# Kernel tuning notes

Hardware: AMD Instinct MI355X
Metric: run time of the kernel (lower is better)

Reference implementation:

```python
import jax, jax.numpy as jnp
import numpy as np

D_MODEL = 1024
D_STATE = 16
D_CONV = 4
EXPAND = 2
D_INNER = EXPAND * D_MODEL          # 2048
DT_RANK = D_INNER // 16             # 128
BATCH = 2
SEQLEN = 1024


def _silu(x):
    return x * jax.nn.sigmoid(x)


def setup_inputs() -> dict:
    key = jax.random.key(0)
    ks = jax.random.split(key, 8)
    s = 0.02
    A_init = jnp.tile(jnp.arange(1, D_STATE + 1, dtype=jnp.float32)[None, :], (D_INNER, 1))
    return {
        "x": jax.random.normal(ks[0], (BATCH, SEQLEN, D_MODEL), jnp.float32),
        "W_in": jax.random.normal(ks[1], (D_MODEL, 2 * D_INNER), jnp.float32) * s,
        "conv_k": jax.random.normal(ks[2], (D_CONV, 1, D_INNER), jnp.float32) * s,  # (kw, in/groups, out)
        "conv_b": jnp.zeros((D_INNER,), jnp.float32),
        "W_xproj": jax.random.normal(ks[3], (D_INNER, DT_RANK + 2 * D_STATE), jnp.float32) * s,
        "W_dt": jax.random.normal(ks[4], (DT_RANK, D_INNER), jnp.float32) * s,
        "b_dt": jnp.zeros((D_INNER,), jnp.float32),
        "A_log": jnp.log(A_init),
        "D": jnp.ones((D_INNER,), jnp.float32),
        "W_out": jax.random.normal(ks[5], (D_INNER, D_MODEL), jnp.float32) * s,
    }


def reference(x, W_in, conv_k, conv_b, W_xproj, W_dt, b_dt, A_log, D, W_out):
    # in_proj and gate split
    xz = x @ W_in                                   # (B, L, 2*Di)
    x_in, z = jnp.split(xz, 2, axis=-1)             # each (B, L, Di)

    # depthwise causal conv1d: left-pad by d_conv-1 (keras padding='causal')
    xp = jnp.pad(x_in, ((0, 0), (D_CONV - 1, 0), (0, 0)))
    x_in = jax.lax.conv_general_dilated(
        xp, conv_k, window_strides=(1,), padding='VALID',
        dimension_numbers=('NWC', 'WIO', 'NWC'),
        feature_group_count=D_INNER) + conv_b
    u = _silu(x_in)                                 # (B, L, Di)

    # input-dependent SSM params
    x_dbl = u @ W_xproj                             # (B, L, dt_rank + 2*N)
    dt_low, Bm, Cm = jnp.split(x_dbl, [DT_RANK, DT_RANK + D_STATE], axis=-1)
    dt = jax.nn.softplus(dt_low @ W_dt + b_dt)      # (B, L, Di)
    A = -jnp.exp(A_log)                             # (Di, N)
    dA = jnp.exp(jnp.einsum('bld,dn->bldn', dt, A)) # (B, L, Di, N)
    dB = jnp.einsum('bld,bln->bldn', dt, Bm)        # (B, L, Di, N)

    # selective scan over sequence length
    def step(h, e):
        a_t, b_t, u_t, c_t = e                      # (B,Di,N), (B,Di,N), (B,Di), (B,N)
        h = a_t * h + b_t * u_t[..., None]
        y_t = jnp.einsum('bdn,bn->bd', h, c_t)
        return h, y_t

    h0 = jnp.zeros((x.shape[0], D_INNER, D_STATE), dtype=x.dtype)
    xs = (jnp.swapaxes(dA, 0, 1), jnp.swapaxes(dB, 0, 1),
          jnp.swapaxes(u, 0, 1), jnp.swapaxes(Cm, 0, 1))
    _, yT = jax.lax.scan(step, h0, xs)              # (L, B, Di)
    y = jnp.swapaxes(yT, 0, 1) + u * D              # skip connection

    return (y * _silu(z)) @ W_out                   # (B, L, d_model)
```

## Files before the change

### kernel.cpp

```cpp
#include <hip/hip_runtime.h>
#include <hip/hip_bf16.h>

#define D_MODEL 1024
#define D_STATE 16
#define D_CONV 4
#define D_INNER 2048
#define DT_RANK 128
#define BATCH 2
#define SEQLEN 1024
#define XCOLS 160
#define NCHUNK 64
#define LCHUNK 16

typedef __hip_bfloat16 bf16;
typedef __attribute__((ext_vector_type(8))) short short8;
typedef __attribute__((ext_vector_type(4))) float f32x4;

__device__ __forceinline__ unsigned short f2bf_bits(float f) {
    bf16 h = __float2bfloat16(f);
    return *(unsigned short*)&h;
}


__global__ __launch_bounds__(256)
void convert_f32_bf16(const float* __restrict__ src, bf16* __restrict__ dst, int n)
{
    int i = blockIdx.x * 256 + threadIdx.x;
    if (i < n) dst[i] = __float2bfloat16(src[i]);
}

__global__ __launch_bounds__(256)
void transpose_f32_bf16(const float* __restrict__ B, bf16* __restrict__ Bt,
                        int K, int N)
{
    __shared__ float t[32][33];
    const int tx = threadIdx.x & 31, ty = threadIdx.x >> 5;
    const int n0 = blockIdx.x * 32, k0 = blockIdx.y * 32;
    #pragma unroll
    for (int r = 0; r < 4; ++r) {
        int k = k0 + ty + r * 8;
        int n = n0 + tx;
        t[ty + r * 8][tx] = (n < N) ? B[(size_t)k * N + n] : 0.f;
    }
    __syncthreads();
    #pragma unroll
    for (int r = 0; r < 4; ++r) {
        int n = n0 + ty + r * 8;
        int k = k0 + tx;
        Bt[(size_t)n * K + k] = __float2bfloat16(t[tx][ty + r * 8]);
    }
}

__global__ __launch_bounds__(256)
void gemm_mfma_bt(const bf16* __restrict__ A, const bf16* __restrict__ Bt,
                  float* __restrict__ C, int M, int N, int K, int ldc, int kchunk)
{
    __shared__ short As[128 * 32];
    __shared__ short Bs[128 * 32];
    const int tid = threadIdx.x;
    const int lane = tid & 63, wave = tid >> 6;
    const int wm = (wave >> 1) * 64, wn = (wave & 1) * 64;
    const int row0 = blockIdx.y * 128, col0 = blockIdx.x * 128;
    const int r_m = lane & 15, r_q = lane >> 4;
    const int kstart = blockIdx.z * kchunk;
    float* Cz = C + (size_t)blockIdx.z * M * ldc;

    const int srow = tid >> 2, schk = (tid & 3) * 8;
    const uint4* Ag0 = (const uint4*)(A  + (size_t)(row0 + srow)      * K + kstart + schk);
    const uint4* Ag1 = (const uint4*)(A  + (size_t)(row0 + srow + 64) * K + kstart + schk);
    const uint4* Bg0 = (const uint4*)(Bt + (size_t)(col0 + srow)      * K + kstart + schk);
    const uint4* Bg1 = (const uint4*)(Bt + (size_t)(col0 + srow + 64) * K + kstart + schk);
    uint4* AsW0 = (uint4*)&As[srow * 32 + schk];
    uint4* AsW1 = (uint4*)&As[(srow + 64) * 32 + schk];
    uint4* BsW0 = (uint4*)&Bs[srow * 32 + schk];
    uint4* BsW1 = (uint4*)&Bs[(srow + 64) * 32 + schk];

    f32x4 acc[4][4];
    #pragma unroll
    for (int i = 0; i < 4; ++i)
        #pragma unroll
        for (int j = 0; j < 4; ++j)
            #pragma unroll
            for (int r = 0; r < 4; ++r) acc[i][j][r] = 0.f;

    for (int k0 = 0; k0 < kchunk; k0 += 32) {
        const int kq = k0 >> 3;
        uint4 a0 = Ag0[kq], a1 = Ag1[kq], b0 = Bg0[kq], b1 = Bg1[kq];
        __syncthreads();
        *AsW0 = a0; *AsW1 = a1; *BsW0 = b0; *BsW1 = b1;
        __syncthreads();
        short8 af[4], bfr[4];
        #pragma unroll
        for (int i = 0; i < 4; ++i)
            af[i] = *(const short8*)&As[(wm + i * 16 + r_m) * 32 + r_q * 8];
        #pragma unroll
        for (int j = 0; j < 4; ++j)
            bfr[j] = *(const short8*)&Bs[(wn + j * 16 + r_m) * 32 + r_q * 8];
        #pragma unroll
        for (int i = 0; i < 4; ++i)
            #pragma unroll
            for (int j = 0; j < 4; ++j)
                acc[i][j] = __builtin_amdgcn_mfma_f32_16x16x32_bf16(
                    af[i], bfr[j], acc[i][j], 0, 0, 0);
    }

    #pragma unroll
    for (int i = 0; i < 4; ++i) {
        #pragma unroll
        for (int j = 0; j < 4; ++j) {
            int row = row0 + wm + i * 16 + r_q * 4;
            int col = col0 + wn + j * 16 + r_m;
            if (col < N) {
                #pragma unroll
                for (int r = 0; r < 4; ++r)
                    Cz[(size_t)(row + r) * ldc + col] = acc[i][j][r];
            }
        }
    }
}

__global__ __launch_bounds__(256)
void reduce_xdbl(const float* __restrict__ Cpart, float* __restrict__ x_dbl,
                 bf16* __restrict__ dtA_bf)
{
    int i = blockIdx.x * 256 + threadIdx.x;
    if (i >= 2048 * XCOLS) return;
    int r = i / XCOLS, c = i - r * XCOLS;
    float s = 0.f;
    #pragma unroll
    for (int z = 0; z < 8; ++z)
        s += Cpart[(size_t)z * 2048 * 256 + (size_t)r * 256 + c];
    x_dbl[i] = s;
    if (c < DT_RANK) dtA_bf[(size_t)r * DT_RANK + c] = __float2bfloat16(s);
}

__global__ __launch_bounds__(256)
void reduce_out(const float* __restrict__ Cpart, float* __restrict__ out)
{
    int i = blockIdx.x * 256 + threadIdx.x;
    const float4* p0 = (const float4*)Cpart;
    const float4* p1 = p0 + (size_t)2048 * 1024 / 4;
    float4 a = p0[i], b = p1[i];
    float4 r; r.x = a.x + b.x; r.y = a.y + b.y; r.z = a.z + b.z; r.w = a.w + b.w;
    ((float4*)out)[i] = r;
}

__global__ __launch_bounds__(256)
void conv_silu_kernel(const float* __restrict__ xz,
                      const float* __restrict__ conv_k,
                      const float* __restrict__ conv_b,
                      float* __restrict__ u, bf16* __restrict__ u_bf)
{
    int idx4 = blockIdx.x * 256 + threadIdx.x;
    int d4 = idx4 & (D_INNER / 4 - 1);
    int t = (idx4 >> 9) & (SEQLEN - 1);
    int b = idx4 >> 19;
    float4 acc = ((const float4*)conv_b)[d4];
    #pragma unroll
    for (int k = 0; k < D_CONV; ++k) {
        int tt = t + k - (D_CONV - 1);
        if (tt >= 0) {
            float4 xv = ((const float4*)xz)[(size_t)(b * SEQLEN + tt) * (2 * D_INNER / 4) + d4];
            float4 kv = ((const float4*)conv_k)[k * (D_INNER / 4) + d4];
            acc.x = fmaf(xv.x, kv.x, acc.x);
            acc.y = fmaf(xv.y, kv.y, acc.y);
            acc.z = fmaf(xv.z, kv.z, acc.z);
            acc.w = fmaf(xv.w, kv.w, acc.w);
        }
    }
    float4 uv;
    uv.x = acc.x / (1.f + __expf(-acc.x));
    uv.y = acc.y / (1.f + __expf(-acc.y));
    uv.z = acc.z / (1.f + __expf(-acc.z));
    uv.w = acc.w / (1.f + __expf(-acc.w));
    ((float4*)u)[idx4] = uv;
    ushort4 pk;
    pk.x = f2bf_bits(uv.x); pk.y = f2bf_bits(uv.y);
    pk.z = f2bf_bits(uv.z); pk.w = f2bf_bits(uv.w);
    ((ushort4*)u_bf)[idx4] = pk;
}

__device__ __forceinline__ float softplus_f(float x) {
    return fmaxf(x, 0.f) + __logf(1.f + __expf(-fabsf(x)));
}

__global__ __launch_bounds__(256)
void scan_phase1(const float* __restrict__ dt_pre,
                 const float* __restrict__ b_dt,
                 const float* __restrict__ A_log,
                 const float* __restrict__ u,
                 const float* __restrict__ x_dbl,
                 float* __restrict__ Pst, float* __restrict__ Sst)
{
    __shared__ float Bsm[LCHUNK][16];
    const int d = blockIdx.x * 256 + threadIdx.x;
    const int c = blockIdx.y, b = blockIdx.z;
    const int t0 = c * LCHUNK;
    {
        int tt = threadIdx.x >> 4, n = threadIdx.x & 15;
        Bsm[tt][n] = x_dbl[(size_t)(b * SEQLEN + t0 + tt) * XCOLS + DT_RANK + n];
    }
    float A_row[D_STATE];
    #pragma unroll
    for (int n = 0; n < D_STATE; ++n)
        A_row[n] = -__expf(A_log[d * D_STATE + n]);
    const float bdt = b_dt[d];
    __syncthreads();
    float P[D_STATE], S[D_STATE];
    #pragma unroll
    for (int n = 0; n < D_STATE; ++n) { P[n] = 1.f; S[n] = 0.f; }
    const float* dpp = dt_pre + (size_t)(b * SEQLEN + t0) * D_INNER + d;
    const float* upp = u + (size_t)(b * SEQLEN + t0) * D_INNER + d;
    #pragma unroll
    for (int t = 0; t < LCHUNK; ++t) {
        float xv = dpp[(size_t)t * D_INNER] + bdt;
        float dtv = softplus_f(xv);
        float du = dtv * upp[(size_t)t * D_INNER];
        const float4* b4 = (const float4*)&Bsm[t][0];
        #pragma unroll
        for (int q = 0; q < 4; ++q) {
            float4 v = b4[q];
            float Bn[4] = {v.x, v.y, v.z, v.w};
            #pragma unroll
            for (int e = 0; e < 4; ++e) {
                int n = q * 4 + e;
                float a = __expf(dtv * A_row[n]);
                P[n] *= a;
                S[n] = fmaf(a, S[n], du * Bn[e]);
            }
        }
    }
    const size_t base = ((size_t)(b * NCHUNK + c) * D_STATE) * D_INNER + d;
    #pragma unroll
    for (int n = 0; n < D_STATE; ++n) {
        Pst[base + (size_t)n * D_INNER] = P[n];
        Sst[base + (size_t)n * D_INNER] = S[n];
    }
}

__global__ __launch_bounds__(256)
void scan_phase2(const float* __restrict__ Pst, float* __restrict__ Sst)
{
    const int d = blockIdx.x * 256 + threadIdx.x;
    const int n = blockIdx.y;
    const int b = blockIdx.z;
    float h = 0.f;
    for (int c = 0; c < NCHUNK; ++c) {
        const size_t idx = ((size_t)(b * NCHUNK + c) * D_STATE + n) * D_INNER + d;
        float Pv = Pst[idx], Sv = Sst[idx];
        Sst[idx] = h;
        h = fmaf(Pv, h, Sv);
    }
}

__global__ __launch_bounds__(256)
void scan_phase3(const float* __restrict__ dt_pre,
                 const float* __restrict__ b_dt,
                 const float* __restrict__ A_log,
                 const float* __restrict__ u,
                 const float* __restrict__ x_dbl,
                 const float* __restrict__ Dvec,
                 const float* __restrict__ xz,
                 const float* __restrict__ hin,
                 bf16* __restrict__ g_bf)
{
    __shared__ float BCs[LCHUNK][32];
    const int d = blockIdx.x * 256 + threadIdx.x;
    const int c = blockIdx.y, b = blockIdx.z;
    const int t0 = c * LCHUNK;
    {
        int i0 = threadIdx.x;
        int tt = i0 >> 5, col = i0 & 31;
        BCs[tt][col] = x_dbl[(size_t)(b * SEQLEN + t0 + tt) * XCOLS + DT_RANK + col];
        int i1 = i0 + 256;
        tt = i1 >> 5; col = i1 & 31;
        BCs[tt][col] = x_dbl[(size_t)(b * SEQLEN + t0 + tt) * XCOLS + DT_RANK + col];
    }
    float A_row[D_STATE];
    #pragma unroll
    for (int n = 0; n < D_STATE; ++n)
        A_row[n] = -__expf(A_log[d * D_STATE + n]);
    const float bdt = b_dt[d];
    const float Dd = Dvec[d];
    __syncthreads();
    float h[D_STATE];
    const size_t base = ((size_t)(b * NCHUNK + c) * D_STATE) * D_INNER + d;
    #pragma unroll
    for (int n = 0; n < D_STATE; ++n) h[n] = hin[base + (size_t)n * D_INNER];
    const float* dpp = dt_pre + (size_t)(b * SEQLEN + t0) * D_INNER + d;
    const float* upp = u + (size_t)(b * SEQLEN + t0) * D_INNER + d;
    const float* zpp = xz + (size_t)(b * SEQLEN + t0) * (2 * D_INNER) + D_INNER + d;
    bf16* gpp = g_bf + (size_t)(b * SEQLEN + t0) * D_INNER + d;
    #pragma unroll
    for (int t = 0; t < LCHUNK; ++t) {
        float xv = dpp[(size_t)t * D_INNER] + bdt;
        float dtv = softplus_f(xv);
        float uv = upp[(size_t)t * D_INNER];
        float zv = zpp[(size_t)t * 2 * D_INNER];
        float du = dtv * uv;
        float y = 0.f;
        const float4* bc4 = (const float4*)&BCs[t][0];
        #pragma unroll
        for (int q = 0; q < 4; ++q) {
            float4 v = bc4[q];
            float4 w = bc4[q + 4];
            float Bn[4] = {v.x, v.y, v.z, v.w};
            float Cn[4] = {w.x, w.y, w.z, w.w};
            #pragma unroll
            for (int e = 0; e < 4; ++e) {
                int n = q * 4 + e;
                float a = __expf(dtv * A_row[n]);
                h[n] = fmaf(a, h[n], du * Bn[e]);
                y = fmaf(h[n], Cn[e], y);
            }
        }
        float gy = y + uv * Dd;
        float sz = zv / (1.f + __expf(-zv));
        gpp[(size_t)t * D_INNER] = __float2bfloat16(gy * sz);
    }
}

extern "C" void kernel_launch(void* const* d_in, const int* in_sizes, int n_in,
                              void* d_out, int out_size, void* d_ws, size_t ws_size,
                              hipStream_t stream)
{
    const float* x      = (const float*)d_in[0];
    const float* W_in   = (const float*)d_in[1];
    const float* conv_k = (const float*)d_in[2];
    const float* conv_b = (const float*)d_in[3];
    const float* W_xproj= (const float*)d_in[4];
    const float* W_dt   = (const float*)d_in[5];
    const float* b_dt   = (const float*)d_in[6];
    const float* A_log  = (const float*)d_in[7];
    const float* Dvec   = (const float*)d_in[8];
    const float* W_out  = (const float*)d_in[9];
    float* out = (float*)d_out;

    const int BL = BATCH * SEQLEN;

    float* ws     = (float*)d_ws;
    float* xz     = ws;
    float* u      = xz     + (size_t)BL * 2 * D_INNER;
    float* x_dbl  = u      + (size_t)BL * D_INNER;
    float* dt_pre = x_dbl  + (size_t)BL * XCOLS;
    float* Pst    = dt_pre + (size_t)BL * D_INNER;
    float* Sst    = Pst    + (size_t)BATCH * NCHUNK * D_STATE * D_INNER;
    float* Cpart3 = Pst;
    float* Cpart6 = Pst;
    bf16*  x_bf   = (bf16*)Sst;
    bf16* Win_t  = (bf16*)(Sst + (size_t)BATCH * NCHUNK * D_STATE * D_INNER);
    bf16* u_bf   = Win_t + (size_t)4096 * 1024;
    bf16* Wxp_t  = u_bf  + (size_t)BL * D_INNER;
    bf16* dtA_bf = Wxp_t + (size_t)256 * 2048;
    bf16* Wdt_t  = dtA_bf+ (size_t)BL * DT_RANK;
    bf16* g_bf   = Wdt_t + (size_t)2048 * 128;
    bf16* Wout_t = g_bf  + (size_t)BL * D_INNER;

    convert_f32_bf16<<<(BL * D_MODEL) / 256, 256, 0, stream>>>(x, x_bf, BL * D_MODEL);
    transpose_f32_bf16<<<dim3(4096 / 32, 1024 / 32), 256, 0, stream>>>(W_in, Win_t, D_MODEL, 2 * D_INNER);
    transpose_f32_bf16<<<dim3(256 / 32, 2048 / 32), 256, 0, stream>>>(W_xproj, Wxp_t, D_INNER, XCOLS);
    transpose_f32_bf16<<<dim3(2048 / 32, 128 / 32), 256, 0, stream>>>(W_dt, Wdt_t, DT_RANK, D_INNER);
    transpose_f32_bf16<<<dim3(1024 / 32, 2048 / 32), 256, 0, stream>>>(W_out, Wout_t, D_INNER, D_MODEL);

    gemm_mfma_bt<<<dim3(32, 16, 1), 256, 0, stream>>>(
        x_bf, Win_t, xz, BL, 2 * D_INNER, D_MODEL, 2 * D_INNER, D_MODEL);

    conv_silu_kernel<<<(BL * D_INNER / 4) / 256, 256, 0, stream>>>(xz, conv_k, conv_b, u, u_bf);

    gemm_mfma_bt<<<dim3(2, 16, 8), 256, 0, stream>>>(
        u_bf, Wxp_t, Cpart3, BL, 256, D_INNER, 256, 256);
    reduce_xdbl<<<(BL * XCOLS + 255) / 256, 256, 0, stream>>>(Cpart3, x_dbl, dtA_bf);

    gemm_mfma_bt<<<dim3(16, 16, 1), 256, 0, stream>>>(
        dtA_bf, Wdt_t, dt_pre, BL, D_INNER, DT_RANK, D_INNER, DT_RANK);

    scan_phase1<<<dim3(D_INNER / 256, NCHUNK, BATCH), 256, 0, stream>>>(
        dt_pre, b_dt, A_log, u, x_dbl, Pst, Sst);
    scan_phase2<<<dim3(D_INNER / 256, D_STATE, BATCH), 256, 0, stream>>>(Pst, Sst);
    scan_phase3<<<dim3(D_INNER / 256, NCHUNK, BATCH), 256, 0, stream>>>(
        dt_pre, b_dt, A_log, u, x_dbl, Dvec, xz, Sst, g_bf);

    gemm_mfma_bt<<<dim3(8, 16, 2), 256, 0, stream>>>(
        g_bf, Wout_t, Cpart6, BL, D_MODEL, D_INNER, D_MODEL, D_MODEL);
    reduce_out<<<(BL * D_MODEL / 4) / 256, 256, 0, stream>>>(Cpart6, out);
}
```

Before: 259.9 us.

## Fuse prep kernels, add softplus GEMM epilogue, direct-to-LDS loads, bf16 u

Merges the input conversion and four weight transposes into one prep kernel that also precomputes -exp(A_log). The dt GEMM now applies the bias and softplus in its epilogue, so the two scan phases no longer recompute them. The GEMMs stage tiles through global_load_lds straight into LDS instead of going through registers. The fp32 copy of u is dropped and the scans read the bf16 u, cutting memory traffic at some precision cost. The new LDS layout writes 8*tid contiguously while the fragment reads assume a row-by-chunk layout; these match because each row takes four 8-element chunks.

```diff
diff --git a/kernel.cpp b/kernel.cpp
--- a/kernel.cpp
+++ b/kernel.cpp
@@ -21,39 +21,86 @@
     return *(unsigned short*)&h;
 }
 
-
-__global__ __launch_bounds__(256)
-void convert_f32_bf16(const float* __restrict__ src, bf16* __restrict__ dst, int n)
-{
-    int i = blockIdx.x * 256 + threadIdx.x;
-    if (i < n) dst[i] = __float2bfloat16(src[i]);
-}
-
-__global__ __launch_bounds__(256)
-void transpose_f32_bf16(const float* __restrict__ B, bf16* __restrict__ Bt,
-                        int K, int N)
+__device__ __forceinline__ float softplus_f(float x) {
+    return fmaxf(x, 0.f) + __logf(1.f + __expf(-fabsf(x)));
+}
+
+__device__ __forceinline__ void load16_lds(void* lds, const void* g) {
+    __builtin_amdgcn_global_load_lds(
+        (const __attribute__((address_space(1))) unsigned int*)g,
+        (__attribute__((address_space(3))) unsigned int*)lds, 16, 0, 0);
+}
+
+__device__ __forceinline__ void transpose_tile(const float* __restrict__ B,
+                                               bf16* __restrict__ Bt,
+                                               int K, int N, int nt, int kt,
+                                               float (*t)[33], int tid)
+{
+    const int tx = tid & 31, ty = tid >> 5;
+    const int n0 = nt * 32, k0 = kt * 32;
+    #pragma unroll
+    for (int r = 0; r < 4; ++r) {
+        int n = n0 + tx;
+        t[ty + r * 8][tx] = (n < N) ? B[(size_t)(k0 + ty + r * 8) * N + n] : 0.f;
+    }
+    __syncthreads();
+    #pragma unroll
+    for (int r = 0; r < 4; ++r)
+        Bt[(size_t)(n0 + ty + r * 8) * K + k0 + tx] = __float2bfloat16(t[tx][ty + r * 8]);
+}
+
+__global__ __launch_bounds__(256)
+void prep_kernel(const float* __restrict__ x, bf16* __restrict__ x_bf,
+                 const float* __restrict__ W_in, bf16* __restrict__ Win_t,
+                 const float* __restrict__ W_xproj, bf16* __restrict__ Wxp_t,
+                 const float* __restrict__ W_dt, bf16* __restrict__ Wdt_t,
+                 const float* __restrict__ W_out, bf16* __restrict__ Wout_t,
+                 const float* __restrict__ A_log, float* __restrict__ Aneg)
 {
     __shared__ float t[32][33];
-    const int tx = threadIdx.x & 31, ty = threadIdx.x >> 5;
-    const int n0 = blockIdx.x * 32, k0 = blockIdx.y * 32;
-    #pragma unroll
-    for (int r = 0; r < 4; ++r) {
-        int k = k0 + ty + r * 8;
-        int n = n0 + tx;
-        t[ty + r * 8][tx] = (n < N) ? B[(size_t)k * N + n] : 0.f;
-    }
-    __syncthreads();
-    #pragma unroll
-    for (int r = 0; r < 4; ++r) {
-        int n = n0 + ty + r * 8;
-        int k = k0 + tx;
-        Bt[(size_t)n * K + k] = __float2bfloat16(t[tx][ty + r * 8]);
-    }
-}
-
+    const int tid = threadIdx.x;
+    int blk = blockIdx.x;
+    if (blk < 4096) {
+        transpose_tile(W_in, Win_t, D_MODEL, 2 * D_INNER, blk & 127, blk >> 7, t, tid);
+        return;
+    }
+    blk -= 4096;
+    if (blk < 512) {
+        transpose_tile(W_xproj, Wxp_t, D_INNER, XCOLS, blk & 7, blk >> 3, t, tid);
+        return;
+    }
+    blk -= 512;
+    if (blk < 256) {
+        transpose_tile(W_dt, Wdt_t, DT_RANK, D_INNER, blk & 63, blk >> 6, t, tid);
+        return;
+    }
+    blk -= 256;
+    if (blk < 2048) {
+        transpose_tile(W_out, Wout_t, D_INNER, D_MODEL, blk & 31, blk >> 5, t, tid);
+        return;
+    }
+    blk -= 2048;
+    if (blk < 2048) {
+        int i = blk * 256 + tid;
+        float4 v = ((const float4*)x)[i];
+        ushort4 p;
+        p.x = f2bf_bits(v.x); p.y = f2bf_bits(v.y);
+        p.z = f2bf_bits(v.z); p.w = f2bf_bits(v.w);
+        ((ushort4*)x_bf)[i] = p;
+        return;
+    }
+    blk -= 2048;
+    {
+        int i = blk * 256 + tid;
+        Aneg[i] = -__expf(A_log[i]);
+    }
+}
+
+template<int EPI>
 __global__ __launch_bounds__(256)
 void gemm_mfma_bt(const bf16* __restrict__ A, const bf16* __restrict__ Bt,
-                  float* __restrict__ C, int M, int N, int K, int ldc, int kchunk)
+                  float* __restrict__ C, const float* __restrict__ bias,
+                  int M, int N, int K, int ldc, int kchunk)
 {
     __shared__ short As[128 * 32];
     __shared__ short Bs[128 * 32];
@@ -66,14 +113,14 @@
     float* Cz = C + (size_t)blockIdx.z * M * ldc;
 
     const int srow = tid >> 2, schk = (tid & 3) * 8;
-    const uint4* Ag0 = (const uint4*)(A  + (size_t)(row0 + srow)      * K + kstart + schk);
-    const uint4* Ag1 = (const uint4*)(A  + (size_t)(row0 + srow + 64) * K + kstart + schk);
-    const uint4* Bg0 = (const uint4*)(Bt + (size_t)(col0 + srow)      * K + kstart + schk);
-    const uint4* Bg1 = (const uint4*)(Bt + (size_t)(col0 + srow + 64) * K + kstart + schk);
-    uint4* AsW0 = (uint4*)&As[srow * 32 + schk];
-    uint4* AsW1 = (uint4*)&As[(srow + 64) * 32 + schk];
-    uint4* BsW0 = (uint4*)&Bs[srow * 32 + schk];
-    uint4* BsW1 = (uint4*)&Bs[(srow + 64) * 32 + schk];
+    const bf16* Ag0 = A  + (size_t)(row0 + srow)      * K + kstart + schk;
+    const bf16* Ag1 = A  + (size_t)(row0 + srow + 64) * K + kstart + schk;
+    const bf16* Bg0 = Bt + (size_t)(col0 + srow)      * K + kstart + schk;
+    const bf16* Bg1 = Bt + (size_t)(col0 + srow + 64) * K + kstart + schk;
+    short* AsW0 = &As[8 * tid];
+    short* AsW1 = &As[8 * tid + 2048];
+    short* BsW0 = &Bs[8 * tid];
+    short* BsW1 = &Bs[8 * tid + 2048];
 
     f32x4 acc[4][4];
     #pragma unroll
@@ -84,10 +131,11 @@
             for (int r = 0; r < 4; ++r) acc[i][j][r] = 0.f;
 
     for (int k0 = 0; k0 < kchunk; k0 += 32) {
-        const int kq = k0 >> 3;
-        uint4 a0 = Ag0[kq], a1 = Ag1[kq], b0 = Bg0[kq], b1 = Bg1[kq];
         __syncthreads();
-        *AsW0 = a0; *AsW1 = a1; *BsW0 = b0; *BsW1 = b1;
+        load16_lds(AsW0, Ag0 + k0);
+        load16_lds(AsW1, Ag1 + k0);
+        load16_lds(BsW0, Bg0 + k0);
+        load16_lds(BsW1, Bg1 + k0);
         __syncthreads();
         short8 af[4], bfr[4];
         #pragma unroll
@@ -111,9 +159,17 @@
             int row = row0 + wm + i * 16 + r_q * 4;
             int col = col0 + wn + j * 16 + r_m;
             if (col < N) {
-                #pragma unroll
-                for (int r = 0; r < 4; ++r)
-                    Cz[(size_t)(row + r) * ldc + col] = acc[i][j][r];
+                if (EPI == 1) {
+                    float bv = bias[col];
+                    #pragma unroll
+                    for (int r = 0; r < 4; ++r)
+                        Cz[(size_t)(row + r) * ldc + col] =
+                            softplus_f(acc[i][j][r] + bv);
+                } else {
+                    #pragma unroll
+                    for (int r = 0; r < 4; ++r)
+                        Cz[(size_t)(row + r) * ldc + col] = acc[i][j][r];
+                }
             }
         }
     }
@@ -149,7 +205,7 @@
 void conv_silu_kernel(const float* __restrict__ xz,
                       const float* __restrict__ conv_k,
                       const float* __restrict__ conv_b,
-                      float* __restrict__ u, bf16* __restrict__ u_bf)
+                      bf16* __restrict__ u_bf)
 {
     int idx4 = blockIdx.x * 256 + threadIdx.x;
     int d4 = idx4 & (D_INNER / 4 - 1);
@@ -168,27 +224,18 @@
             acc.w = fmaf(xv.w, kv.w, acc.w);
         }
     }
-    float4 uv;
-    uv.x = acc.x / (1.f + __expf(-acc.x));
-    uv.y = acc.y / (1.f + __expf(-acc.y));
-    uv.z = acc.z / (1.f + __expf(-acc.z));
-    uv.w = acc.w / (1.f + __expf(-acc.w));
-    ((float4*)u)[idx4] = uv;
     ushort4 pk;
-    pk.x = f2bf_bits(uv.x); pk.y = f2bf_bits(uv.y);
-    pk.z = f2bf_bits(uv.z); pk.w = f2bf_bits(uv.w);
+    pk.x = f2bf_bits(acc.x / (1.f + __expf(-acc.x)));
+    pk.y = f2bf_bits(acc.y / (1.f + __expf(-acc.y)));
+    pk.z = f2bf_bits(acc.z / (1.f + __expf(-acc.z)));
+    pk.w = f2bf_bits(acc.w / (1.f + __expf(-acc.w)));
     ((ushort4*)u_bf)[idx4] = pk;
 }
 
-__device__ __forceinline__ float softplus_f(float x) {
-    return fmaxf(x, 0.f) + __logf(1.f + __expf(-fabsf(x)));
-}
-
-__global__ __launch_bounds__(256)
-void scan_phase1(const float* __restrict__ dt_pre,
-                 const float* __restrict__ b_dt,
-                 const float* __restrict__ A_log,
-                 const float* __restrict__ u,
+__global__ __launch_bounds__(256)
+void scan_phase1(const float* __restrict__ dt_s,
+                 const float* __restrict__ Aneg,
+                 const bf16* __restrict__ u_bf,
                  const float* __restrict__ x_dbl,
                  float* __restrict__ Pst, float* __restrict__ Sst)
 {
@@ -201,21 +248,22 @@
         Bsm[tt][n] = x_dbl[(size_t)(b * SEQLEN + t0 + tt) * XCOLS + DT_RANK + n];
     }
     float A_row[D_STATE];
-    #pragma unroll
-    for (int n = 0; n < D_STATE; ++n)
-        A_row[n] = -__expf(A_log[d * D_STATE + n]);
-    const float bdt = b_dt[d];
+    const float4* a4 = (const float4*)(Aneg + d * D_STATE);
+    #pragma unroll
+    for (int q = 0; q < 4; ++q) {
+        float4 v = a4[q];
+        A_row[q*4+0] = v.x; A_row[q*4+1] = v.y; A_row[q*4+2] = v.z; A_row[q*4+3] = v.w;
+    }
     __syncthreads();
     float P[D_STATE], S[D_STATE];
     #pragma unroll
     for (int n = 0; n < D_STATE; ++n) { P[n] = 1.f; S[n] = 0.f; }
-    const float* dpp = dt_pre + (size_t)(b * SEQLEN + t0) * D_INNER + d;
-    const float* upp = u + (size_t)(b * SEQLEN + t0) * D_INNER + d;
+    const float* dpp = dt_s + (size_t)(b * SEQLEN + t0) * D_INNER + d;
+    const bf16* upp = u_bf + (size_t)(b * SEQLEN + t0) * D_INNER + d;
     #pragma unroll
     for (int t = 0; t < LCHUNK; ++t) {
-        float xv = dpp[(size_t)t * D_INNER] + bdt;
-        float dtv = softplus_f(xv);
-        float du = dtv * upp[(size_t)t * D_INNER];
+        float dtv = dpp[(size_t)t * D_INNER];
+        float du = dtv * __bfloat162float(upp[(size_t)t * D_INNER]);
         const float4* b4 = (const float4*)&Bsm[t][0];
         #pragma unroll
         for (int q = 0; q < 4; ++q) {
@@ -254,10 +302,9 @@
 }
 
 __global__ __launch_bounds__(256)
-void scan_phase3(const float* __restrict__ dt_pre,
-                 const float* __restrict__ b_dt,
-                 const float* __restrict__ A_log,
-                 const float* __restrict__ u,
+void scan_phase3(const float* __restrict__ dt_s,
+                 const float* __restrict__ Aneg,
+                 const bf16* __restrict__ u_bf,
                  const float* __restrict__ x_dbl,
                  const float* __restrict__ Dvec,
                  const float* __restrict__ xz,
@@ -277,25 +324,26 @@
         BCs[tt][col] = x_dbl[(size_t)(b * SEQLEN + t0 + tt) * XCOLS + DT_RANK + col];
     }
     float A_row[D_STATE];
-    #pragma unroll
-    for (int n = 0; n < D_STATE; ++n)
-        A_row[n] = -__expf(A_log[d * D_STATE + n]);
-    const float bdt = b_dt[d];
+    const float4* a4 = (const float4*)(Aneg + d * D_STATE);
+    #pragma unroll
+    for (int q = 0; q < 4; ++q) {
+        float4 v = a4[q];
+        A_row[q*4+0] = v.x; A_row[q*4+1] = v.y; A_row[q*4+2] = v.z; A_row[q*4+3] = v.w;
+    }
     const float Dd = Dvec[d];
     __syncthreads();
     float h[D_STATE];
     const size_t base = ((size_t)(b * NCHUNK + c) * D_STATE) * D_INNER + d;
     #pragma unroll
     for (int n = 0; n < D_STATE; ++n) h[n] = hin[base + (size_t)n * D_INNER];
-    const float* dpp = dt_pre + (size_t)(b * SEQLEN + t0) * D_INNER + d;
-    const float* upp = u + (size_t)(b * SEQLEN + t0) * D_INNER + d;
+    const float* dpp = dt_s + (size_t)(b * SEQLEN + t0) * D_INNER + d;
+    const bf16* upp = u_bf + (size_t)(b * SEQLEN + t0) * D_INNER + d;
     const float* zpp = xz + (size_t)(b * SEQLEN + t0) * (2 * D_INNER) + D_INNER + d;
     bf16* gpp = g_bf + (size_t)(b * SEQLEN + t0) * D_INNER + d;
     #pragma unroll
     for (int t = 0; t < LCHUNK; ++t) {
-        float xv = dpp[(size_t)t * D_INNER] + bdt;
-        float dtv = softplus_f(xv);
-        float uv = upp[(size_t)t * D_INNER];
+        float dtv = dpp[(size_t)t * D_INNER];
+        float uv = __bfloat162float(upp[(size_t)t * D_INNER]);
         float zv = zpp[(size_t)t * 2 * D_INNER];
         float du = dtv * uv;
         float y = 0.f;
@@ -340,15 +388,15 @@
 
     float* ws     = (float*)d_ws;
     float* xz     = ws;
-    float* u      = xz     + (size_t)BL * 2 * D_INNER;
-    float* x_dbl  = u      + (size_t)BL * D_INNER;
-    float* dt_pre = x_dbl  + (size_t)BL * XCOLS;
-    float* Pst    = dt_pre + (size_t)BL * D_INNER;
+    float* x_dbl  = xz     + (size_t)BL * 2 * D_INNER;
+    float* dt_s   = x_dbl  + (size_t)BL * XCOLS;
+    float* Pst    = dt_s   + (size_t)BL * D_INNER;
     float* Sst    = Pst    + (size_t)BATCH * NCHUNK * D_STATE * D_INNER;
+    float* Aneg   = Sst    + (size_t)BATCH * NCHUNK * D_STATE * D_INNER;
     float* Cpart3 = Pst;
     float* Cpart6 = Pst;
     bf16*  x_bf   = (bf16*)Sst;
-    bf16* Win_t  = (bf16*)(Sst + (size_t)BATCH * NCHUNK * D_STATE * D_INNER);
+    bf16* Win_t  = (bf16*)(Aneg + 32768);
     bf16* u_bf   = Win_t + (size_t)4096 * 1024;
     bf16* Wxp_t  = u_bf  + (size_t)BL * D_INNER;
     bf16* dtA_bf = Wxp_t + (size_t)256 * 2048;
@@ -356,31 +404,28 @@
     bf16* g_bf   = Wdt_t + (size_t)2048 * 128;
     bf16* Wout_t = g_bf  + (size_t)BL * D_INNER;
 
-    convert_f32_bf16<<<(BL * D_MODEL) / 256, 256, 0, stream>>>(x, x_bf, BL * D_MODEL);
-    transpose_f32_bf16<<<dim3(4096 / 32, 1024 / 32), 256, 0, stream>>>(W_in, Win_t, D_MODEL, 2 * D_INNER);
-    transpose_f32_bf16<<<dim3(256 / 32, 2048 / 32), 256, 0, stream>>>(W_xproj, Wxp_t, D_INNER, XCOLS);
-    transpose_f32_bf16<<<dim3(2048 / 32, 128 / 32), 256, 0, stream>>>(W_dt, Wdt_t, DT_RANK, D_INNER);
-    transpose_f32_bf16<<<dim3(1024 / 32, 2048 / 32), 256, 0, stream>>>(W_out, Wout_t, D_INNER, D_MODEL);
-
-    gemm_mfma_bt<<<dim3(32, 16, 1), 256, 0, stream>>>(
-        x_bf, Win_t, xz, BL, 2 * D_INNER, D_MODEL, 2 * D_INNER, D_MODEL);
-
-    conv_silu_kernel<<<(BL * D_INNER / 4) / 256, 256, 0, stream>>>(xz, conv_k, conv_b, u, u_bf);
-
-    gemm_mfma_bt<<<dim3(2, 16, 8), 256, 0, stream>>>(
-        u_bf, Wxp_t, Cpart3, BL, 256, D_INNER, 256, 256);
+    prep_kernel<<<4096 + 512 + 256 + 2048 + 2048 + 128, 256, 0, stream>>>(
+        x, x_bf, W_in, Win_t, W_xproj, Wxp_t, W_dt, Wdt_t, W_out, Wout_t, A_log, Aneg);
+
+    gemm_mfma_bt<0><<<dim3(32, 16, 1), 256, 0, stream>>>(
+        x_bf, Win_t, xz, nullptr, BL, 2 * D_INNER, D_MODEL, 2 * D_INNER, D_MODEL);
+
+    conv_silu_kernel<<<(BL * D_INNER / 4) / 256, 256, 0, stream>>>(xz, conv_k, conv_b, u_bf);
+
+    gemm_mfma_bt<0><<<dim3(2, 16, 8), 256, 0, stream>>>(
+        u_bf, Wxp_t, Cpart3, nullptr, BL, 256, D_INNER, 256, 256);
     reduce_xdbl<<<(BL * XCOLS + 255) / 256, 256, 0, stream>>>(Cpart3, x_dbl, dtA_bf);
 
-    gemm_mfma_bt<<<dim3(16, 16, 1), 256, 0, stream>>>(
-        dtA_bf, Wdt_t, dt_pre, BL, D_INNER, DT_RANK, D_INNER, DT_RANK);
+    gemm_mfma_bt<1><<<dim3(16, 16, 1), 256, 0, stream>>>(
+        dtA_bf, Wdt_t, dt_s, b_dt, BL, D_INNER, DT_RANK, D_INNER, DT_RANK);
 
     scan_phase1<<<dim3(D_INNER / 256, NCHUNK, BATCH), 256, 0, stream>>>(
-        dt_pre, b_dt, A_log, u, x_dbl, Pst, Sst);
+        dt_s, Aneg, u_bf, x_dbl, Pst, Sst);
     scan_phase2<<<dim3(D_INNER / 256, D_STATE, BATCH), 256, 0, stream>>>(Pst, Sst);
     scan_phase3<<<dim3(D_INNER / 256, NCHUNK, BATCH), 256, 0, stream>>>(
-        dt_pre, b_dt, A_log, u, x_dbl, Dvec, xz, Sst, g_bf);
-
-    gemm_mfma_bt<<<dim3(8, 16, 2), 256, 0, stream>>>(
-        g_bf, Wout_t, Cpart6, BL, D_MODEL, D_INNER, D_MODEL, D_MODEL);
+        dt_s, Aneg, u_bf, x_dbl, Dvec, xz, Sst, g_bf);
+
+    gemm_mfma_bt<0><<<dim3(8, 16, 2), 256, 0, stream>>>(
+        g_bf, Wout_t, Cpart6, nullptr, BL, D_MODEL, D_INNER, D_MODEL, D_MODEL);
     reduce_out<<<(BL * D_MODEL / 4) / 256, 256, 0, stream>>>(Cpart6, out);
 }
```

Measured after the change: 244.3 us. 6.0% less time.
